# Performance work log

Measured on AMD Instinct MI355X. Metric: run time of the kernel, lower is better.

The kernel has to match this reference:

```python
import jax, jax.numpy as jnp
import numpy as np
import math

B, S, D = 2, 2048, 1024
H, DK, DV = 16, 64, 64  # head_count, query_size, value_size; H*DV == D
NEG_INF = -jnp.inf


def setup_inputs() -> dict:
    key = jax.random.key(0)
    ks = jax.random.split(key, 10)
    sc = 0.02
    return {
        "input": jax.random.normal(ks[0], (B, S, D), dtype=jnp.float32),
        "padding_mask": jnp.zeros((B, S), dtype=jnp.float32),  # 0 = valid, 1 = padded
        "wq_w": jax.random.normal(ks[1], (H * DK, D), dtype=jnp.float32) * sc,
        "wq_b": jnp.zeros((H * DK,), dtype=jnp.float32),
        "wk_w": jax.random.normal(ks[2], (H * DK, D), dtype=jnp.float32) * sc,
        "wk_b": jnp.zeros((H * DK,), dtype=jnp.float32),
        "wv_w": jax.random.normal(ks[3], (H * DV, D), dtype=jnp.float32) * sc,
        "wv_b": jnp.zeros((H * DV,), dtype=jnp.float32),
        "fin_w": jax.random.normal(ks[4], (D, H * DV), dtype=jnp.float32) * sc,
        "fin_b": jnp.zeros((D,), dtype=jnp.float32),
    }


def reference(input, padding_mask, wq_w, wq_b, wk_w, wk_b, wv_w, wv_b, fin_w, fin_b):
    b, s, _ = input.shape
    # projections -> [b, h, s, d]
    Q = (input @ wq_w.T + wq_b).reshape(b, s, H, DK).transpose(0, 2, 1, 3)
    K = (input @ wk_w.T + wk_b).reshape(b, s, H, DK).transpose(0, 2, 1, 3)
    V = (input @ wv_w.T + wv_b).reshape(b, s, H, DV).transpose(0, 2, 1, 3)

    # padding mask: pad*(-inf), nan_to_num(0*inf -> 0); broadcast over query dim
    pad = jnp.where(padding_mask > 0, NEG_INF, 0.0)[:, None, None, :]  # [b,1,1,s]
    i = jnp.arange(s)
    causal = jnp.where(i[None, :] < i[:, None] + 1, 0.0, NEG_INF)  # [s,s]
    mask = pad + causal[None, None, :, :]

    # (QK^T + mask) / sqrt(dk), softmax over keys
    logits = (jnp.einsum("bhqd,bhkd->bhqk", Q, K) + mask) / math.sqrt(DK)
    attn = jax.nn.softmax(logits, axis=-1)
    out = jnp.einsum("bhqk,bhkd->bqhd", attn, V).reshape(b, s, H * DV)
    return out @ fin_w.T + fin_b
```

## Files before the change

### kernel.cpp

```cpp
#include <hip/hip_runtime.h>


typedef __bf16 bf16;
typedef __bf16 bf16x8 __attribute__((ext_vector_type(8)));
typedef __bf16 bf16x4 __attribute__((ext_vector_type(4)));
typedef float  f32x4  __attribute__((ext_vector_type(4)));

#define B_  2
#define S_  2048
#define D_  1024
#define H_  16
#define HD  64
#define NEG_BIG (-3.0e38f)
#define SCALE_LOG2E 0.1803368801111204f

__device__ __forceinline__ void lds16(const void* g, void* l) {
    __builtin_amdgcn_global_load_lds((const __attribute__((address_space(1))) void*)g,
                                     (__attribute__((address_space(3))) void*)l, 16, 0, 0);
}

__device__ __forceinline__ f32x4 mfma16(bf16x8 a, bf16x8 b, f32x4 c) {
    return __builtin_amdgcn_mfma_f32_16x16x32_bf16(a, b, c, 0, 0, 0);
}

__global__ __launch_bounds__(256) void convert_k(const float* __restrict__ X,
                                                 const float* __restrict__ wq,
                                                 const float* __restrict__ wk,
                                                 const float* __restrict__ wv,
                                                 const float* __restrict__ wo,
                                                 bf16* __restrict__ dst) {
    const int gid = blockIdx.x * 256 + threadIdx.x;
    const int i   = gid * 4;
    const float* src;
    int off;
    if      (i < (4 << 20)) { src = X;  off = 0; }
    else if (i < (5 << 20)) { src = wq; off = 4 << 20; }
    else if (i < (6 << 20)) { src = wk; off = 5 << 20; }
    else if (i < (7 << 20)) { src = wv; off = 6 << 20; }
    else                    { src = wo; off = 7 << 20; }
    const float4 v = *(const float4*)(src + (i - off));
    bf16x4 p;
    p[0] = (bf16)v.x; p[1] = (bf16)v.y; p[2] = (bf16)v.z; p[3] = (bf16)v.w;
    *(bf16x4*)(dst + i) = p;
}

__global__ __launch_bounds__(256) void gemm_qkv(const bf16* __restrict__ A,
                                                const bf16* __restrict__ Wq,
                                                const bf16* __restrict__ Wk,
                                                const bf16* __restrict__ Wv,
                                                const float* __restrict__ bq,
                                                const float* __restrict__ bk,
                                                const float* __restrict__ bv,
                                                bf16* __restrict__ Qw,
                                                bf16* __restrict__ Kw,
                                                bf16* __restrict__ Vw) {
    constexpr int K = 1024;
    __shared__ bf16 sA[128 * 32];
    __shared__ bf16 sB[128 * 32];
    const int tid  = threadIdx.x;
    const int l15  = tid & 15;
    const int quad = (tid & 63) >> 4;
    const int wid  = tid >> 6;
    const int seg  = blockIdx.x >> 3;
    const int bn   = blockIdx.x & 7;
    const int bm   = blockIdx.y;
    const int wm   = (wid >> 1) * 64;
    const int wn   = (wid & 1) * 64;

    const bf16* W    = (seg == 0) ? Wq : (seg == 1) ? Wk : Wv;
    const float* bias = (seg == 0) ? bq : (seg == 1) ? bk : bv;

    const bf16* Ab = A + (size_t)bm * 128 * K;
    const bf16* Wb = W + (size_t)bn * 128 * K;

    f32x4 acc[4][4] = {};

    for (int k0 = 0; k0 < K; k0 += 32) {
        __syncthreads();
        #pragma unroll
        for (int it = 0; it < 2; ++it) {
            int c = it * 256 + tid;
            int row = c >> 2, c8 = c & 3;
            lds16(Ab + row * K + k0 + c8 * 8, (char*)sA + c * 16);
            lds16(Wb + row * K + k0 + c8 * 8, (char*)sB + c * 16);
        }
        __syncthreads();
        bf16x8 af[4], bfr[4];
        #pragma unroll
        for (int i = 0; i < 4; ++i)
            af[i] = *(const bf16x8*)&sA[(wm + i * 16 + l15) * 32 + quad * 8];
        #pragma unroll
        for (int i = 0; i < 4; ++i)
            bfr[i] = *(const bf16x8*)&sB[(wn + i * 16 + l15) * 32 + quad * 8];
        #pragma unroll
        for (int mi = 0; mi < 4; ++mi)
            #pragma unroll
            for (int ni = 0; ni < 4; ++ni)
                acc[mi][ni] = mfma16(af[mi], bfr[ni], acc[mi][ni]);
    }

    #pragma unroll
    for (int ni = 0; ni < 4; ++ni) {
        const int n  = bn * 128 + wn + ni * 16 + l15;
        const float bv_ = bias[n];
        const int h = n >> 6;
        #pragma unroll
        for (int mi = 0; mi < 4; ++mi) {
            const int m0 = bm * 128 + wm + mi * 16 + quad * 4;
            if (seg == 2) {
                const int dv = n & 63;
                const int b = m0 >> 11, s = m0 & 2047;
                bf16x4 pack;
                #pragma unroll
                for (int r = 0; r < 4; ++r) pack[r] = (bf16)(acc[mi][ni][r] + bv_);
                *(bf16x4*)&Vw[(((size_t)(b * H_ + h) * HD + dv) << 11) + s] = pack;
            } else {
                bf16* C = (seg == 0) ? Qw : Kw;
                const int dk = n & 63;
                #pragma unroll
                for (int r = 0; r < 4; ++r) {
                    const int m = m0 + r, b = m >> 11, s = m & 2047;
                    C[(((size_t)(b * H_ + h) << 11) + s) * HD + dk] =
                        (bf16)(acc[mi][ni][r] + bv_);
                }
            }
        }
    }
}

__global__ __launch_bounds__(256) void gemm_fin(const bf16* __restrict__ A,
                                                const bf16* __restrict__ W,
                                                const float* __restrict__ bias,
                                                float* __restrict__ C) {
    constexpr int N = 1024, K = 1024;
    __shared__ bf16 sA[128 * 32];
    __shared__ bf16 sB[128 * 32];
    const int tid  = threadIdx.x;
    const int l15  = tid & 15;
    const int quad = (tid & 63) >> 4;
    const int wid  = tid >> 6;
    const int bm   = blockIdx.x >> 3;
    const int bn   = blockIdx.x & 7;
    const int wm   = (wid >> 1) * 64;
    const int wn   = (wid & 1) * 64;

    const bf16* Ab = A + (size_t)bm * 128 * K;
    const bf16* Wb = W + (size_t)bn * 128 * K;

    f32x4 acc[4][4] = {};

    for (int k0 = 0; k0 < K; k0 += 32) {
        __syncthreads();
        #pragma unroll
        for (int it = 0; it < 2; ++it) {
            int c = it * 256 + tid;
            int row = c >> 2, c8 = c & 3;
            lds16(Ab + row * K + k0 + c8 * 8, (char*)sA + c * 16);
            lds16(Wb + row * K + k0 + c8 * 8, (char*)sB + c * 16);
        }
        __syncthreads();
        bf16x8 af[4], bfr[4];
        #pragma unroll
        for (int i = 0; i < 4; ++i)
            af[i] = *(const bf16x8*)&sA[(wm + i * 16 + l15) * 32 + quad * 8];
        #pragma unroll
        for (int i = 0; i < 4; ++i)
            bfr[i] = *(const bf16x8*)&sB[(wn + i * 16 + l15) * 32 + quad * 8];
        #pragma unroll
        for (int mi = 0; mi < 4; ++mi)
            #pragma unroll
            for (int ni = 0; ni < 4; ++ni)
                acc[mi][ni] = mfma16(af[mi], bfr[ni], acc[mi][ni]);
    }

    #pragma unroll
    for (int ni = 0; ni < 4; ++ni) {
        const int n  = bn * 128 + wn + ni * 16 + l15;
        const float bv = bias[n];
        #pragma unroll
        for (int mi = 0; mi < 4; ++mi) {
            const int m0 = bm * 128 + wm + mi * 16 + quad * 4;
            #pragma unroll
            for (int r = 0; r < 4; ++r)
                C[(size_t)(m0 + r) * N + n] = acc[mi][ni][r] + bv;
        }
    }
}

#define PSTRIDE 136
__global__ __launch_bounds__(512, 4) void attn_k(const bf16* __restrict__ Q,
                                                 const bf16* __restrict__ K,
                                                 const bf16* __restrict__ Vt,
                                                 const float* __restrict__ pmask,
                                                 bf16* __restrict__ Aout) {
    __shared__ bf16 sK_[2 * 128 * 32];
    __shared__ bf16 sV[4 * 64 * 32];
    __shared__ bf16 sP[128 * PSTRIDE];
    const int tid  = threadIdx.x;
    const int l15  = tid & 15;
    const int quad = (tid & 63) >> 4;
    const int wid  = tid >> 6;
    const int idx  = blockIdx.x >> 5;
    const int qt   = (idx < 8) ? (15 - idx) : (idx - 8);
    const int bh   = blockIdx.x & 31;
    const int b    = bh >> 4;
    const int h    = bh & 15;

    const bf16* Qg = Q + ((size_t)bh * S_ + qt * 128) * HD;
    #pragma unroll
    for (int it = 0; it < 2; ++it) {
        int c = it * 512 + tid;
        int pl = c >> 9, row = (c >> 2) & 127, c8 = c & 3;
        lds16(Qg + row * HD + pl * 32 + c8 * 8, (char*)sP + c * 16);
    }
    bf16x8 kreg[2], vreg[2];
    {
        const bf16* Kg = K  + (size_t)bh * S_ * HD;
        const bf16* Vg = Vt + (size_t)bh * HD * S_;
        #pragma unroll
        for (int it = 0; it < 2; ++it) {
            int c = it * 512 + tid;
            int pl = c >> 9, row = (c >> 2) & 127, c8 = c & 3;
            kreg[it] = *(const bf16x8*)(Kg + row * HD + pl * 32 + c8 * 8);
            int kc = c >> 8, dv = (c >> 2) & 63;
            vreg[it] = *(const bf16x8*)(Vg + dv * S_ + kc * 32 + c8 * 8);
        }
    }
    __syncthreads();
    bf16x8 aq[2];
    #pragma unroll
    for (int kk = 0; kk < 2; ++kk)
        aq[kk] = *(const bf16x8*)&sP[(kk * 128 + wid * 16 + l15) * 32 + quad * 8];

    float m_i = NEG_BIG, l_i = 0.f;
    f32x4 o[4] = {};
    const int qg = wid * 16 + l15;

    for (int kt = 0; kt <= qt; ++kt) {
        __syncthreads();
        #pragma unroll
        for (int it = 0; it < 2; ++it) {
            int c = it * 512 + tid;
            *(bf16x8*)((char*)sK_ + c * 16) = kreg[it];
            *(bf16x8*)((char*)sV  + c * 16) = vreg[it];
        }
        if (kt < qt) {
            const bf16* Kg = K  + ((size_t)bh * S_ + (kt + 1) * 128) * HD;
            const bf16* Vg = Vt + (size_t)bh * HD * S_ + (kt + 1) * 128;
            #pragma unroll
            for (int it = 0; it < 2; ++it) {
                int c = it * 512 + tid;
                int pl = c >> 9, row = (c >> 2) & 127, c8 = c & 3;
                kreg[it] = *(const bf16x8*)(Kg + row * HD + pl * 32 + c8 * 8);
                int kc = c >> 8, dv = (c >> 2) & 63;
                vreg[it] = *(const bf16x8*)(Vg + dv * S_ + kc * 32 + c8 * 8);
            }
        }
        __syncthreads();

        f32x4 s[8] = {};
        #pragma unroll
        for (int tc = 0; tc < 8; ++tc) {
            #pragma unroll
            for (int kk = 0; kk < 2; ++kk) {
                bf16x8 kb = *(const bf16x8*)
                    &sK_[(kk * 128 + tc * 16 + l15) * 32 + quad * 8];
                s[tc] = mfma16(kb, aq[kk], s[tc]);
            }
        }

        const bool diag = (kt == qt);
        #pragma unroll
        for (int tc = 0; tc < 8; ++tc) {
            const float4 pv = *(const float4*)
                &pmask[b * S_ + kt * 128 + tc * 16 + quad * 4];
            #pragma unroll
            for (int r = 0; r < 4; ++r) {
                float v = s[tc][r] * SCALE_LOG2E;
                if (((const float*)&pv)[r] > 0.f) v = NEG_BIG;
                if (diag && (tc * 16 + quad * 4 + r > qg)) v = NEG_BIG;
                s[tc][r] = v;
            }
        }

        float rm = s[0][0];
        #pragma unroll
        for (int tc = 0; tc < 8; ++tc)
            #pragma unroll
            for (int r = 0; r < 4; ++r) rm = fmaxf(rm, s[tc][r]);
        rm = fmaxf(rm, __shfl_xor(rm, 16));
        rm = fmaxf(rm, __shfl_xor(rm, 32));
        const float mn    = fmaxf(m_i, rm);
        const float alpha = exp2f(m_i - mn);
        m_i = mn;
        float rs = 0.f;
        #pragma unroll
        for (int tc = 0; tc < 8; ++tc)
            #pragma unroll
            for (int r = 0; r < 4; ++r) {
                float p = exp2f(s[tc][r] - mn);
                s[tc][r] = p;
                rs += p;
            }
        rs += __shfl_xor(rs, 16);
        rs += __shfl_xor(rs, 32);
        l_i = l_i * alpha + rs;

        #pragma unroll
        for (int tc = 0; tc < 8; ++tc) {
            bf16x4 pk;
            #pragma unroll
            for (int r = 0; r < 4; ++r) pk[r] = (bf16)s[tc][r];
            *(bf16x4*)&sP[qg * PSTRIDE + tc * 16 + quad * 4] = pk;
        }

        #pragma unroll
        for (int r = 0; r < 4; ++r) {
            float ar = __shfl(alpha, quad * 4 + r, 16);
            #pragma unroll
            for (int vc = 0; vc < 4; ++vc) o[vc][r] *= ar;
        }
        __syncthreads();

        #pragma unroll
        for (int kc = 0; kc < 4; ++kc) {
            bf16x8 ap = *(const bf16x8*)
                &sP[(wid * 16 + l15) * PSTRIDE + kc * 32 + quad * 8];
            #pragma unroll
            for (int vc = 0; vc < 4; ++vc) {
                bf16x8 bv = *(const bf16x8*)
                    &sV[(kc * 64 + vc * 16 + l15) * 32 + quad * 8];
                o[vc] = mfma16(ap, bv, o[vc]);
            }
        }
    }

    const float inv = 1.f / l_i;
    #pragma unroll
    for (int r = 0; r < 4; ++r) {
        float ir = __shfl(inv, quad * 4 + r, 16);
        int q = qt * 128 + wid * 16 + quad * 4 + r;
        size_t base = ((size_t)b * S_ + q) * D_ + h * HD;
        #pragma unroll
        for (int vc = 0; vc < 4; ++vc)
            Aout[base + vc * 16 + l15] = (bf16)(o[vc][r] * ir);
    }
}

extern "C" void kernel_launch(void* const* d_in, const int* in_sizes, int n_in,
                              void* d_out, int out_size, void* d_ws, size_t ws_size,
                              hipStream_t stream) {
    const float* X   = (const float*)d_in[0];
    const float* pm  = (const float*)d_in[1];
    const float* wq  = (const float*)d_in[2];
    const float* bq  = (const float*)d_in[3];
    const float* wk  = (const float*)d_in[4];
    const float* bk  = (const float*)d_in[5];
    const float* wv  = (const float*)d_in[6];
    const float* bvb = (const float*)d_in[7];
    const float* wo  = (const float*)d_in[8];
    const float* bo  = (const float*)d_in[9];
    float* out = (float*)d_out;

    char* ws = (char*)d_ws;
    bf16* Xb  = (bf16*)(ws);
    bf16* Wqb = (bf16*)(ws + (8u  << 20));
    bf16* Wkb = (bf16*)(ws + (10u << 20));
    bf16* Wvb = (bf16*)(ws + (12u << 20));
    bf16* Wob = (bf16*)(ws + (14u << 20));
    bf16* Qw  = (bf16*)(ws + (16u << 20));
    bf16* Kw  = (bf16*)(ws + (24u << 20));
    bf16* Vw  = (bf16*)(ws + (32u << 20));
    bf16* Aw  = (bf16*)(ws + (40u << 20));

    convert_k<<<dim3(8192), dim3(256), 0, stream>>>(X, wq, wk, wv, wo, Xb);
    gemm_qkv<<<dim3(24, 32), dim3(256), 0, stream>>>(Xb, Wqb, Wkb, Wvb,
                                                     bq, bk, bvb, Qw, Kw, Vw);
    attn_k<<<dim3(512), dim3(512), 0, stream>>>(Qw, Kw, Vw, pm, Aw);
    gemm_fin<<<dim3(256), dim3(256), 0, stream>>>(Aw, Wob, bo, out);
}
```

Measured before the change: 224.3 us.

## Rewrite attention as per-wave 32-row register flash kernel with 32x32 MFMA

Attention is rewritten so each wave owns a 32-query tile and works independently. Q, K and V are loaded directly from global memory into registers and multiplied with 32x32x16 MFMA, so the LDS staging and block-wide barriers go away. P is passed between the two MFMAs through lane shuffles instead of shared memory. Waves pair a short and a long causal row range for load balance. The output GEMM tile also shrinks to 64x128 to launch twice as many blocks. The costs are more redundant global K/V traffic, since waves no longer share tiles, and higher register pressure.

Result: slower. 266.5 us (+18.8%).

```diff
diff --git a/kernel.cpp b/kernel.cpp
--- a/kernel.cpp
+++ b/kernel.cpp
@@ -2,9 +2,11 @@
 
 
 typedef __bf16 bf16;
+typedef __bf16 bf16x2 __attribute__((ext_vector_type(2)));
+typedef __bf16 bf16x4 __attribute__((ext_vector_type(4)));
 typedef __bf16 bf16x8 __attribute__((ext_vector_type(8)));
-typedef __bf16 bf16x4 __attribute__((ext_vector_type(4)));
 typedef float  f32x4  __attribute__((ext_vector_type(4)));
+typedef float  f32x16 __attribute__((ext_vector_type(16)));
 
 #define B_  2
 #define S_  2048
@@ -21,6 +23,14 @@
 
 __device__ __forceinline__ f32x4 mfma16(bf16x8 a, bf16x8 b, f32x4 c) {
     return __builtin_amdgcn_mfma_f32_16x16x32_bf16(a, b, c, 0, 0, 0);
+}
+__device__ __forceinline__ f32x16 mfma32(bf16x8 a, bf16x8 b, f32x16 c) {
+    return __builtin_amdgcn_mfma_f32_32x32x16_bf16(a, b, c, 0, 0, 0);
+}
+__device__ __forceinline__ int pk2(float a, float b) {
+    union { bf16x2 h; int i; } u;
+    u.h[0] = (bf16)a; u.h[1] = (bf16)b;
+    return u.i;
 }
 
 __global__ __launch_bounds__(256) void convert_k(const float* __restrict__ X,
@@ -133,7 +143,7 @@
                                                 const float* __restrict__ bias,
                                                 float* __restrict__ C) {
     constexpr int N = 1024, K = 1024;
-    __shared__ bf16 sA[128 * 32];
+    __shared__ bf16 sA[64 * 32];
     __shared__ bf16 sB[128 * 32];
     const int tid  = threadIdx.x;
     const int l15  = tid & 15;
@@ -141,33 +151,36 @@
     const int wid  = tid >> 6;
     const int bm   = blockIdx.x >> 3;
     const int bn   = blockIdx.x & 7;
-    const int wm   = (wid >> 1) * 64;
-    const int wn   = (wid & 1) * 64;
-
-    const bf16* Ab = A + (size_t)bm * 128 * K;
+    const int wm   = (wid & 1) * 32;
+    const int wn   = (wid >> 1) * 64;
+
+    const bf16* Ab = A + (size_t)bm * 64 * K;
     const bf16* Wb = W + (size_t)bn * 128 * K;
 
-    f32x4 acc[4][4] = {};
+    f32x4 acc[2][4] = {};
 
     for (int k0 = 0; k0 < K; k0 += 32) {
         __syncthreads();
+        {
+            int c = tid, row = c >> 2, c8 = c & 3;
+            lds16(Ab + row * K + k0 + c8 * 8, (char*)sA + c * 16);
+        }
         #pragma unroll
         for (int it = 0; it < 2; ++it) {
             int c = it * 256 + tid;
             int row = c >> 2, c8 = c & 3;
-            lds16(Ab + row * K + k0 + c8 * 8, (char*)sA + c * 16);
             lds16(Wb + row * K + k0 + c8 * 8, (char*)sB + c * 16);
         }
         __syncthreads();
-        bf16x8 af[4], bfr[4];
-        #pragma unroll
-        for (int i = 0; i < 4; ++i)
+        bf16x8 af[2], bfr[4];
+        #pragma unroll
+        for (int i = 0; i < 2; ++i)
             af[i] = *(const bf16x8*)&sA[(wm + i * 16 + l15) * 32 + quad * 8];
         #pragma unroll
         for (int i = 0; i < 4; ++i)
             bfr[i] = *(const bf16x8*)&sB[(wn + i * 16 + l15) * 32 + quad * 8];
         #pragma unroll
-        for (int mi = 0; mi < 4; ++mi)
+        for (int mi = 0; mi < 2; ++mi)
             #pragma unroll
             for (int ni = 0; ni < 4; ++ni)
                 acc[mi][ni] = mfma16(af[mi], bfr[ni], acc[mi][ni]);
@@ -178,8 +191,8 @@
         const int n  = bn * 128 + wn + ni * 16 + l15;
         const float bv = bias[n];
         #pragma unroll
-        for (int mi = 0; mi < 4; ++mi) {
-            const int m0 = bm * 128 + wm + mi * 16 + quad * 4;
+        for (int mi = 0; mi < 2; ++mi) {
+            const int m0 = bm * 64 + wm + mi * 16 + quad * 4;
             #pragma unroll
             for (int r = 0; r < 4; ++r)
                 C[(size_t)(m0 + r) * N + n] = acc[mi][ni][r] + bv;
@@ -187,164 +200,178 @@
     }
 }
 
-#define PSTRIDE 136
-__global__ __launch_bounds__(512, 4) void attn_k(const bf16* __restrict__ Q,
+template <int NS>
+__device__ __forceinline__ void attn_group(
+    int sub0, int s, int l31, int hi,
+    const bf16* __restrict__ Kg, const bf16* __restrict__ Vg,
+    const float* __restrict__ pmg,
+    const bf16x8 (&qf)[4], bf16x8 (&kf)[2][4],
+    float& m_i, float& l_i, f32x16 (&ot)[2], int nsubT)
+{
+    f32x16 st[NS] = {};
+    #pragma unroll
+    for (int su = 0; su < NS; ++su)
+        #pragma unroll
+        for (int ks = 0; ks < 4; ++ks)
+            st[su] = mfma32(kf[su][ks], qf[ks], st[su]);
+
+    bf16x8 vf[2][NS][2];
+    #pragma unroll
+    for (int t = 0; t < 2; ++t)
+        #pragma unroll
+        for (int su = 0; su < NS; ++su)
+            #pragma unroll
+            for (int k2 = 0; k2 < 2; ++k2)
+                vf[t][su][k2] = *(const bf16x8*)
+                    (Vg + (size_t)(t * 32 + l31) * S_ + (sub0 + su) * 32 + k2 * 16 + hi * 8);
+
+    float4 pmv[NS][4];
+    #pragma unroll
+    for (int su = 0; su < NS; ++su)
+        #pragma unroll
+        for (int rg = 0; rg < 4; ++rg)
+            pmv[su][rg] = *(const float4*)(pmg + (sub0 + su) * 32 + rg * 8 + hi * 4);
+
+    {
+        const int nxt = sub0 + NS;
+        const int nrem = nsubT - nxt;
+        if (nrem > 0) {
+            #pragma unroll
+            for (int ks = 0; ks < 4; ++ks)
+                kf[0][ks] = *(const bf16x8*)
+                    (Kg + (size_t)(nxt * 32 + l31) * HD + ks * 16 + hi * 8);
+            if (nrem > 1)
+                #pragma unroll
+                for (int ks = 0; ks < 4; ++ks)
+                    kf[1][ks] = *(const bf16x8*)
+                        (Kg + (size_t)((nxt + 1) * 32 + l31) * HD + ks * 16 + hi * 8);
+        }
+    }
+
+    float sv[NS][16];
+    const int thr = l31 - 4 * hi;
+    #pragma unroll
+    for (int su = 0; su < NS; ++su) {
+        const bool dg = (sub0 + su == s);
+        #pragma unroll
+        for (int rg = 0; rg < 4; ++rg) {
+            const float4 pf = pmv[su][rg];
+            #pragma unroll
+            for (int e = 0; e < 4; ++e) {
+                const int r = rg * 4 + e;
+                float v = st[su][r] * SCALE_LOG2E;
+                if (((const float*)&pf)[e] > 0.f) v = NEG_BIG;
+                if (dg && (e + 8 * rg > thr)) v = NEG_BIG;
+                sv[su][r] = v;
+            }
+        }
+    }
+
+    float rm = sv[0][0];
+    #pragma unroll
+    for (int su = 0; su < NS; ++su)
+        #pragma unroll
+        for (int r = 0; r < 16; ++r) rm = fmaxf(rm, sv[su][r]);
+    rm = fmaxf(rm, __shfl_xor(rm, 32));
+    const float mn    = fmaxf(m_i, rm);
+    const float alpha = exp2f(m_i - mn);
+    m_i = mn;
+    float rs = 0.f;
+    #pragma unroll
+    for (int su = 0; su < NS; ++su)
+        #pragma unroll
+        for (int r = 0; r < 16; ++r) {
+            const float p = exp2f(sv[su][r] - mn);
+            sv[su][r] = p;
+            rs += p;
+        }
+    rs += __shfl_xor(rs, 32);
+    l_i = l_i * alpha + rs;
+    ot[0] *= alpha;
+    ot[1] *= alpha;
+
+    #pragma unroll
+    for (int su = 0; su < NS; ++su) {
+        int P[8], X[8];
+        #pragma unroll
+        for (int i = 0; i < 8; ++i) {
+            P[i] = pk2(sv[su][2 * i], sv[su][2 * i + 1]);
+            X[i] = __shfl_xor(P[i], 32);
+        }
+        union { int d[4]; bf16x8 v; } f0, f1;
+        if (hi == 0) {
+            f0.d[0] = P[0]; f0.d[1] = P[1]; f0.d[2] = X[0]; f0.d[3] = X[1];
+            f1.d[0] = P[4]; f1.d[1] = P[5]; f1.d[2] = X[4]; f1.d[3] = X[5];
+        } else {
+            f0.d[0] = X[2]; f0.d[1] = X[3]; f0.d[2] = P[2]; f0.d[3] = P[3];
+            f1.d[0] = X[6]; f1.d[1] = X[7]; f1.d[2] = P[6]; f1.d[3] = P[7];
+        }
+        #pragma unroll
+        for (int t = 0; t < 2; ++t) {
+            ot[t] = mfma32(vf[t][su][0], f0.v, ot[t]);
+            ot[t] = mfma32(vf[t][su][1], f1.v, ot[t]);
+        }
+    }
+}
+
+__global__ __launch_bounds__(256, 2) void attn_k(const bf16* __restrict__ Q,
                                                  const bf16* __restrict__ K,
                                                  const bf16* __restrict__ Vt,
                                                  const float* __restrict__ pmask,
                                                  bf16* __restrict__ Aout) {
-    __shared__ bf16 sK_[2 * 128 * 32];
-    __shared__ bf16 sV[4 * 64 * 32];
-    __shared__ bf16 sP[128 * PSTRIDE];
-    const int tid  = threadIdx.x;
-    const int l15  = tid & 15;
-    const int quad = (tid & 63) >> 4;
-    const int wid  = tid >> 6;
-    const int idx  = blockIdx.x >> 5;
-    const int qt   = (idx < 8) ? (15 - idx) : (idx - 8);
+    const int lane = threadIdx.x & 63;
+    const int l31  = lane & 31;
+    const int hi   = lane >> 5;
+    const int wid  = threadIdx.x >> 6;
+    const int jj   = blockIdx.x >> 5;
     const int bh   = blockIdx.x & 31;
     const int b    = bh >> 4;
     const int h    = bh & 15;
-
-    const bf16* Qg = Q + ((size_t)bh * S_ + qt * 128) * HD;
-    #pragma unroll
-    for (int it = 0; it < 2; ++it) {
-        int c = it * 512 + tid;
-        int pl = c >> 9, row = (c >> 2) & 127, c8 = c & 3;
-        lds16(Qg + row * HD + pl * 32 + c8 * 8, (char*)sP + c * 16);
-    }
-    bf16x8 kreg[2], vreg[2];
+    const int s = (wid < 2) ? (2 * jj + wid)
+                            : ((wid == 2) ? (62 - 2 * jj) : (63 - 2 * jj));
+    const int nsubT = s + 1;
+
+    const bf16* Qg = Q  + ((size_t)bh * S_ + s * 32) * HD;
+    const bf16* Kg = K  + (size_t)bh * S_ * HD;
+    const bf16* Vg = Vt + (size_t)bh * HD * S_;
+    const float* pmg = pmask + b * S_;
+
+    bf16x8 qf[4];
+    #pragma unroll
+    for (int ks = 0; ks < 4; ++ks)
+        qf[ks] = *(const bf16x8*)(Qg + l31 * HD + ks * 16 + hi * 8);
+
+    bf16x8 kf[2][4];
     {
-        const bf16* Kg = K  + (size_t)bh * S_ * HD;
-        const bf16* Vg = Vt + (size_t)bh * HD * S_;
-        #pragma unroll
-        for (int it = 0; it < 2; ++it) {
-            int c = it * 512 + tid;
-            int pl = c >> 9, row = (c >> 2) & 127, c8 = c & 3;
-            kreg[it] = *(const bf16x8*)(Kg + row * HD + pl * 32 + c8 * 8);
-            int kc = c >> 8, dv = (c >> 2) & 63;
-            vreg[it] = *(const bf16x8*)(Vg + dv * S_ + kc * 32 + c8 * 8);
-        }
-    }
-    __syncthreads();
-    bf16x8 aq[2];
-    #pragma unroll
-    for (int kk = 0; kk < 2; ++kk)
-        aq[kk] = *(const bf16x8*)&sP[(kk * 128 + wid * 16 + l15) * 32 + quad * 8];
+        const int n0 = (nsubT < 2) ? nsubT : 2;
+        for (int su = 0; su < n0; ++su)
+            #pragma unroll
+            for (int ks = 0; ks < 4; ++ks)
+                kf[su][ks] = *(const bf16x8*)
+                    (Kg + (size_t)(su * 32 + l31) * HD + ks * 16 + hi * 8);
+    }
 
     float m_i = NEG_BIG, l_i = 0.f;
-    f32x4 o[4] = {};
-    const int qg = wid * 16 + l15;
-
-    for (int kt = 0; kt <= qt; ++kt) {
-        __syncthreads();
-        #pragma unroll
-        for (int it = 0; it < 2; ++it) {
-            int c = it * 512 + tid;
-            *(bf16x8*)((char*)sK_ + c * 16) = kreg[it];
-            *(bf16x8*)((char*)sV  + c * 16) = vreg[it];
-        }
-        if (kt < qt) {
-            const bf16* Kg = K  + ((size_t)bh * S_ + (kt + 1) * 128) * HD;
-            const bf16* Vg = Vt + (size_t)bh * HD * S_ + (kt + 1) * 128;
-            #pragma unroll
-            for (int it = 0; it < 2; ++it) {
-                int c = it * 512 + tid;
-                int pl = c >> 9, row = (c >> 2) & 127, c8 = c & 3;
-                kreg[it] = *(const bf16x8*)(Kg + row * HD + pl * 32 + c8 * 8);
-                int kc = c >> 8, dv = (c >> 2) & 63;
-                vreg[it] = *(const bf16x8*)(Vg + dv * S_ + kc * 32 + c8 * 8);
-            }
-        }
-        __syncthreads();
-
-        f32x4 s[8] = {};
-        #pragma unroll
-        for (int tc = 0; tc < 8; ++tc) {
-            #pragma unroll
-            for (int kk = 0; kk < 2; ++kk) {
-                bf16x8 kb = *(const bf16x8*)
-                    &sK_[(kk * 128 + tc * 16 + l15) * 32 + quad * 8];
-                s[tc] = mfma16(kb, aq[kk], s[tc]);
-            }
-        }
-
-        const bool diag = (kt == qt);
-        #pragma unroll
-        for (int tc = 0; tc < 8; ++tc) {
-            const float4 pv = *(const float4*)
-                &pmask[b * S_ + kt * 128 + tc * 16 + quad * 4];
-            #pragma unroll
-            for (int r = 0; r < 4; ++r) {
-                float v = s[tc][r] * SCALE_LOG2E;
-                if (((const float*)&pv)[r] > 0.f) v = NEG_BIG;
-                if (diag && (tc * 16 + quad * 4 + r > qg)) v = NEG_BIG;
-                s[tc][r] = v;
-            }
-        }
-
-        float rm = s[0][0];
-        #pragma unroll
-        for (int tc = 0; tc < 8; ++tc)
-            #pragma unroll
-            for (int r = 0; r < 4; ++r) rm = fmaxf(rm, s[tc][r]);
-        rm = fmaxf(rm, __shfl_xor(rm, 16));
-        rm = fmaxf(rm, __shfl_xor(rm, 32));
-        const float mn    = fmaxf(m_i, rm);
-        const float alpha = exp2f(m_i - mn);
-        m_i = mn;
-        float rs = 0.f;
-        #pragma unroll
-        for (int tc = 0; tc < 8; ++tc)
-            #pragma unroll
-            for (int r = 0; r < 4; ++r) {
-                float p = exp2f(s[tc][r] - mn);
-                s[tc][r] = p;
-                rs += p;
-            }
-        rs += __shfl_xor(rs, 16);
-        rs += __shfl_xor(rs, 32);
-        l_i = l_i * alpha + rs;
-
-        #pragma unroll
-        for (int tc = 0; tc < 8; ++tc) {
-            bf16x4 pk;
-            #pragma unroll
-            for (int r = 0; r < 4; ++r) pk[r] = (bf16)s[tc][r];
-            *(bf16x4*)&sP[qg * PSTRIDE + tc * 16 + quad * 4] = pk;
-        }
-
-        #pragma unroll
-        for (int r = 0; r < 4; ++r) {
-            float ar = __shfl(alpha, quad * 4 + r, 16);
-            #pragma unroll
-            for (int vc = 0; vc < 4; ++vc) o[vc][r] *= ar;
-        }
-        __syncthreads();
-
-        #pragma unroll
-        for (int kc = 0; kc < 4; ++kc) {
-            bf16x8 ap = *(const bf16x8*)
-                &sP[(wid * 16 + l15) * PSTRIDE + kc * 32 + quad * 8];
-            #pragma unroll
-            for (int vc = 0; vc < 4; ++vc) {
-                bf16x8 bv = *(const bf16x8*)
-                    &sV[(kc * 64 + vc * 16 + l15) * 32 + quad * 8];
-                o[vc] = mfma16(ap, bv, o[vc]);
-            }
-        }
-    }
+    f32x16 ot[2] = {};
+
+    const int full = nsubT >> 1;
+    for (int g = 0; g < full; ++g)
+        attn_group<2>(g * 2, s, l31, hi, Kg, Vg, pmg, qf, kf, m_i, l_i, ot, nsubT);
+    if (nsubT & 1)
+        attn_group<1>(nsubT - 1, s, l31, hi, Kg, Vg, pmg, qf, kf, m_i, l_i, ot, nsubT);
 
     const float inv = 1.f / l_i;
-    #pragma unroll
-    for (int r = 0; r < 4; ++r) {
-        float ir = __shfl(inv, quad * 4 + r, 16);
-        int q = qt * 128 + wid * 16 + quad * 4 + r;
-        size_t base = ((size_t)b * S_ + q) * D_ + h * HD;
-        #pragma unroll
-        for (int vc = 0; vc < 4; ++vc)
-            Aout[base + vc * 16 + l15] = (bf16)(o[vc][r] * ir);
-    }
+    const int q = s * 32 + l31;
+    bf16* outp = Aout + ((size_t)b * S_ + q) * D_ + h * HD;
+    #pragma unroll
+    for (int t = 0; t < 2; ++t)
+        #pragma unroll
+        for (int rg = 0; rg < 4; ++rg) {
+            bf16x4 pv;
+            #pragma unroll
+            for (int e = 0; e < 4; ++e) pv[e] = (bf16)(ot[t][rg * 4 + e] * inv);
+            *(bf16x4*)(outp + t * 32 + rg * 8 + hi * 4) = pv;
+        }
 }
 
 extern "C" void kernel_launch(void* const* d_in, const int* in_sizes, int n_in,
@@ -376,6 +403,6 @@
     convert_k<<<dim3(8192), dim3(256), 0, stream>>>(X, wq, wk, wv, wo, Xb);
     gemm_qkv<<<dim3(24, 32), dim3(256), 0, stream>>>(Xb, Wqb, Wkb, Wvb,
                                                      bq, bk, bvb, Qw, Kw, Vw);
-    attn_k<<<dim3(512), dim3(512), 0, stream>>>(Qw, Kw, Vw, pm, Aw);
-    gemm_fin<<<dim3(256), dim3(256), 0, stream>>>(Aw, Wob, bo, out);
-}
+    attn_k<<<dim3(512), dim3(256), 0, stream>>>(Qw, Kw, Vw, pm, Aw);
+    gemm_fin<<<dim3(512), dim3(256), 0, stream>>>(Aw, Wob, bo, out);
+}
```
